# Optimization experiments

Measured on AMD Instinct MI355X. Metric: run time of the kernel, lower is better.

Reference implementation:

```python
import jax, jax.numpy as jnp
import numpy as np

NEG_BIG = -1e30  # stand-in for -inf in the log-space eps state


def wkv_scan(w, u, k, v, alpha0, beta0, eps0):
    """Numerically-stable RWKV WKV recurrence.

    w: exp(time_decay) (D,), u: time_first (D,)
    k, v: (B, T, D); alpha0, beta0, eps0: (B, D)
    Returns wkv (B, T, D) and final state.
    """
    def step(carry, kv_t):
        alpha, beta, eps = carry
        kt, vt = kv_t  # (B, D)
        # output: (e^{u+k} v + alpha) / (e^{u+k} + beta), stabilized
        ww = u + kt
        tau = jnp.maximum(eps, ww)
        e1 = jnp.exp(eps - tau)
        e2 = jnp.exp(ww - tau)
        out = (e1 * alpha + e2 * vt) / (e1 * beta + e2)
        # state update with decay: alpha' = e^{-w} alpha + e^{k} v (log-space)
        ww2 = eps - w
        tau2 = jnp.maximum(ww2, kt)
        e1b = jnp.exp(ww2 - tau2)
        e2b = jnp.exp(kt - tau2)
        return (e1b * alpha + e2b * vt, e1b * beta + e2b, tau2), out

    kT = jnp.swapaxes(k, 0, 1)  # (T, B, D)
    vT = jnp.swapaxes(v, 0, 1)
    (_, _, _), outs = jax.lax.scan(step, (alpha0, beta0, eps0), (kT, vT))
    return jnp.swapaxes(outs, 0, 1)  # (B, T, D)


def setup_inputs() -> dict:
    key = jax.random.key(0)
    ks = jax.random.split(key, 10)
    B, T, D = 4, 2048, 2048
    scale = 1.0 / np.sqrt(D)
    x = jax.random.normal(ks[0], (B, T, D), dtype=jnp.float32)
    time_decay = jax.random.uniform(ks[1], (D,), minval=-1.0, maxval=1.0)
    time_first = 0.1 * jax.random.normal(ks[2], (D,))
    time_mix_k = jax.random.uniform(ks[3], (1, 1, D))
    time_mix_v = jax.random.uniform(ks[4], (1, 1, D))
    time_mix_r = jax.random.uniform(ks[5], (1, 1, D))
    Wk = scale * jax.random.normal(ks[6], (D, D))
    Wv = scale * jax.random.normal(ks[7], (D, D))
    Wr = scale * jax.random.normal(ks[8], (D, D))
    Wo = scale * jax.random.normal(ks[9], (D, D))
    return {"x": x, "time_decay": time_decay, "time_first": time_first,
            "time_mix_k": time_mix_k, "time_mix_v": time_mix_v,
            "time_mix_r": time_mix_r, "Wk": Wk, "Wv": Wv, "Wr": Wr, "Wo": Wo}


def reference(x, time_decay, time_first, time_mix_k, time_mix_v, time_mix_r,
              Wk, Wv, Wr, Wo):
    B, T, D = x.shape
    # time_shift: prepend zero init_x, drop last token
    last_x = jnp.concatenate([jnp.zeros((B, 1, D), x.dtype), x[:, :-1, :]], axis=1)
    k = jnp.einsum('btd,ed->bte', x * time_mix_k + last_x * (1 - time_mix_k), Wk)
    v = jnp.einsum('btd,ed->bte', x * time_mix_v + last_x * (1 - time_mix_v), Wv)
    r = jnp.einsum('btd,ed->bte', x * time_mix_r + last_x * (1 - time_mix_r), Wr)
    sr = jax.nn.sigmoid(r)
    w = jnp.exp(time_decay)
    alpha0 = jnp.zeros((B, D), x.dtype)
    beta0 = jnp.zeros((B, D), x.dtype)
    eps0 = jnp.full((B, D), NEG_BIG, x.dtype)
    wkv = wkv_scan(w, time_first, k, v, alpha0, beta0, eps0)
    return jnp.einsum('btd,ed->bte', wkv * sr, Wo)
```

## Files before the change

### kernel.cpp

```cpp
#include <hip/hip_runtime.h>
#include <stdint.h>

typedef __bf16 bf16x8 __attribute__((ext_vector_type(8)));
typedef float f32x4 __attribute__((ext_vector_type(4)));

#define BM 128
#define BN 128
#define BK 64

__global__ void cvt_bf16(const float* __restrict__ in, __bf16* __restrict__ out,
                         long n) {
    long idx = ((long)blockIdx.x * blockDim.x + threadIdx.x) * 8;
    if (idx >= n) return;
    f32x4 a = *(const f32x4*)(in + idx);
    f32x4 b = *(const f32x4*)(in + idx + 4);
    bf16x8 o;
#pragma unroll
    for (int i = 0; i < 4; ++i) { o[i] = (__bf16)a[i]; o[i + 4] = (__bf16)b[i]; }
    *(bf16x8*)(out + idx) = o;
}

__global__ void mix_kernel(const float* __restrict__ x,
                           const float* __restrict__ mixw,
                           __bf16* __restrict__ out,
                           int T, int D, long total) {
    long idx = ((long)blockIdx.x * blockDim.x + threadIdx.x) * 8;
    if (idx >= total) return;
    int d = (int)(idx % D);
    long bt = idx / D;
    int t = (int)(bt % T);

    f32x4 x0 = *(const f32x4*)(x + idx);
    f32x4 x1 = *(const f32x4*)(x + idx + 4);
    f32x4 l0 = {}, l1 = {};
    if (t != 0) {
        l0 = *(const f32x4*)(x + idx - D);
        l1 = *(const f32x4*)(x + idx - D + 4);
    }
    f32x4 m0 = *(const f32x4*)(mixw + d);
    f32x4 m1 = *(const f32x4*)(mixw + d + 4);
    bf16x8 o;
#pragma unroll
    for (int i = 0; i < 4; ++i) {
        o[i]     = (__bf16)(x0[i] * m0[i] + l0[i] * (1.0f - m0[i]));
        o[i + 4] = (__bf16)(x1[i] * m1[i] + l1[i] * (1.0f - m1[i]));
    }
    *(bf16x8*)(out + idx) = o;
}

template <typename CT>
__global__ __launch_bounds__(256, 3)
void gemm_bt(const __bf16* __restrict__ A, const __bf16* __restrict__ Bt,
             CT* __restrict__ C, int M, int N, int K) {
    __shared__ __align__(16) __bf16 sA[BM * BK];
    __shared__ __align__(16) __bf16 sB[BN * BK];

    const int tid  = threadIdx.x;
    const int lane = tid & 63;
    const int wave = tid >> 6;
    const int m0 = blockIdx.y * BM;
    const int n0 = blockIdx.x * BN;
    const int wm = (wave & 1) * 64;
    const int wn = (wave >> 1) * 64;

    const int l8 = lane >> 3;
    const int c8 = lane & 7;
    const int cg = c8 ^ l8;

    const int q  = lane >> 4;
    const int ml = lane & 15;

    f32x4 acc[4][4] = {};

    for (int k0 = 0; k0 < K; k0 += BK) {
#pragma unroll
        for (int i = 0; i < 4; ++i) {
            const int cl  = wave * 4 + i;
            const int row = cl * 8 + l8;
            const __bf16* gA = A  + (long)(m0 + row) * K + (k0 + cg * 8);
            const __bf16* gB = Bt + (long)(n0 + row) * K + (k0 + cg * 8);
            __builtin_amdgcn_global_load_lds(
                (const __attribute__((address_space(1))) void*)gA,
                (__attribute__((address_space(3))) void*)(sA + cl * 512), 16, 0, 0);
            __builtin_amdgcn_global_load_lds(
                (const __attribute__((address_space(1))) void*)gB,
                (__attribute__((address_space(3))) void*)(sB + cl * 512), 16, 0, 0);
        }
        __syncthreads();

#pragma unroll
        for (int kk = 0; kk < BK; kk += 32) {
            bf16x8 af[4], bfr[4];
#pragma unroll
            for (int i = 0; i < 4; ++i) {
                int row = wm + i * 16 + ml;
                int cl  = ((kk >> 3) + q) ^ (row & 7);
                af[i] = *(const bf16x8*)(sA + row * BK + cl * 8);
            }
#pragma unroll
            for (int j = 0; j < 4; ++j) {
                int row = wn + j * 16 + ml;
                int cl  = ((kk >> 3) + q) ^ (row & 7);
                bfr[j] = *(const bf16x8*)(sB + row * BK + cl * 8);
            }
#pragma unroll
            for (int i = 0; i < 4; ++i)
#pragma unroll
                for (int j = 0; j < 4; ++j)
                    acc[i][j] = __builtin_amdgcn_mfma_f32_16x16x32_bf16(
                        af[i], bfr[j], acc[i][j], 0, 0, 0);
        }
        __syncthreads();
    }

#pragma unroll
    for (int i = 0; i < 4; ++i)
#pragma unroll
        for (int j = 0; j < 4; ++j)
#pragma unroll
            for (int rg = 0; rg < 4; ++rg) {
                int row = m0 + wm + i * 16 + q * 4 + rg;
                int col = n0 + wn + j * 16 + ml;
                C[(long)row * N + col] = (CT)acc[i][j][rg];
            }
}

template <typename ST>
__global__ void wkv_pass1(const ST* __restrict__ kk, const ST* __restrict__ vv,
                          const float* __restrict__ td,
                          float* __restrict__ al, float* __restrict__ bl,
                          float* __restrict__ el,
                          int Bn, int T, int D, int C, int L) {
    int gid = blockIdx.x * blockDim.x + threadIdx.x;
    int BD = Bn * D;
    if (gid >= BD * C) return;
    int c  = gid / BD;
    int bd = gid - c * BD;
    int b  = bd / D;
    int d  = bd - b * D;

    float w = __expf(td[d]);
    float alpha = 0.f, beta = 0.f, eps = -1e30f;
    long base = ((long)b * T + (long)c * L) * D + d;

    const int P = 8;
    float kb0[P], vb0[P], kb1[P], vb1[P];

    auto step = [&](float kt, float vt) {
        float ww2  = eps - w;
        float tau2 = fmaxf(ww2, kt);
        float e1b  = __expf(ww2 - tau2);
        float e2b  = __expf(kt - tau2);
        alpha = e1b * alpha + e2b * vt;
        beta  = e1b * beta + e2b;
        eps   = tau2;
    };

#pragma unroll
    for (int j = 0; j < P; ++j) {
        long o = base + (long)j * D;
        kb0[j] = (float)kk[o]; vb0[j] = (float)vv[o];
    }
    for (int t0 = 0; t0 < L; t0 += 2 * P) {
#pragma unroll
        for (int j = 0; j < P; ++j) {
            long o = base + (long)(t0 + P + j) * D;
            kb1[j] = (float)kk[o]; vb1[j] = (float)vv[o];
        }
#pragma unroll
        for (int j = 0; j < P; ++j) step(kb0[j], vb0[j]);
        if (t0 + 2 * P < L) {
#pragma unroll
            for (int j = 0; j < P; ++j) {
                long o = base + (long)(t0 + 2 * P + j) * D;
                kb0[j] = (float)kk[o]; vb0[j] = (float)vv[o];
            }
        }
#pragma unroll
        for (int j = 0; j < P; ++j) step(kb1[j], vb1[j]);
    }
    al[gid] = alpha; bl[gid] = beta; el[gid] = eps;
}

__global__ void wkv_combine(const float* __restrict__ al, const float* __restrict__ bl,
                            const float* __restrict__ el, const float* __restrict__ td,
                            float* __restrict__ ai, float* __restrict__ bi,
                            float* __restrict__ ei,
                            int Bn, int D, int C, int L) {
    int bd = blockIdx.x * blockDim.x + threadIdx.x;
    int BD = Bn * D;
    if (bd >= BD) return;
    int d = bd % D;
    float wL = __expf(td[d]) * (float)L;
    float a = 0.f, b2 = 0.f, e = -1e30f;
    for (int c = 0; c < C; ++c) {
        int idx = c * BD + bd;
        ai[idx] = a; bi[idx] = b2; ei[idx] = e;
        float ed  = e - wL;
        float la = al[idx], lb = bl[idx], le = el[idx];
        float tau = fmaxf(ed, le);
        float e1  = __expf(ed - tau);
        float e2  = __expf(le - tau);
        a  = a * e1 + la * e2;
        b2 = b2 * e1 + lb * e2;
        e  = tau;
    }
}

template <typename ST>
__global__ void wkv_pass2(const ST* __restrict__ kk, const ST* __restrict__ vv,
                          const __bf16* __restrict__ rr,
                          const float* __restrict__ td, const float* __restrict__ tf,
                          const float* __restrict__ ai, const float* __restrict__ bi,
                          const float* __restrict__ ei,
                          __bf16* __restrict__ out,
                          int Bn, int T, int D, int C, int L) {
    int gid = blockIdx.x * blockDim.x + threadIdx.x;
    int BD = Bn * D;
    if (gid >= BD * C) return;
    int c  = gid / BD;
    int bd = gid - c * BD;
    int b  = bd / D;
    int d  = bd - b * D;

    float u = tf[d];
    float w = __expf(td[d]);
    float alpha = ai[gid], beta = bi[gid], eps = ei[gid];
    long base = ((long)b * T + (long)c * L) * D + d;

    const int P = 8;
    float kb0[P], vb0[P], rb0[P], kb1[P], vb1[P], rb1[P];

    auto step = [&](float kt, float vt, float rt, int tIdx) {
        float ww  = u + kt;
        float tau = fmaxf(eps, ww);
        float e1  = __expf(eps - tau);
        float e2  = __expf(ww - tau);
        float num = e1 * alpha + e2 * vt;
        float den = e1 * beta + e2;
        float o_  = num * __builtin_amdgcn_rcpf(den);
        float ww2  = eps - w;
        float tau2 = fmaxf(ww2, kt);
        float e1b  = __expf(ww2 - tau2);
        float e2b  = __expf(kt - tau2);
        alpha = e1b * alpha + e2b * vt;
        beta  = e1b * beta + e2b;
        eps   = tau2;
        float sr = __builtin_amdgcn_rcpf(1.0f + __expf(-rt));
        out[base + (long)tIdx * D] = (__bf16)(o_ * sr);
    };

#pragma unroll
    for (int j = 0; j < P; ++j) {
        long o = base + (long)j * D;
        kb0[j] = (float)kk[o]; vb0[j] = (float)vv[o]; rb0[j] = (float)rr[o];
    }
    for (int t0 = 0; t0 < L; t0 += 2 * P) {
#pragma unroll
        for (int j = 0; j < P; ++j) {
            long o = base + (long)(t0 + P + j) * D;
            kb1[j] = (float)kk[o]; vb1[j] = (float)vv[o]; rb1[j] = (float)rr[o];
        }
#pragma unroll
        for (int j = 0; j < P; ++j) step(kb0[j], vb0[j], rb0[j], t0 + j);
        if (t0 + 2 * P < L) {
#pragma unroll
            for (int j = 0; j < P; ++j) {
                long o = base + (long)(t0 + 2 * P + j) * D;
                kb0[j] = (float)kk[o]; vb0[j] = (float)vv[o]; rb0[j] = (float)rr[o];
            }
        }
#pragma unroll
        for (int j = 0; j < P; ++j) step(kb1[j], vb1[j], rb1[j], t0 + P + j);
    }
}

extern "C" void kernel_launch(void* const* d_in, const int* in_sizes, int n_in,
                              void* d_out, int out_size, void* d_ws, size_t ws_size,
                              hipStream_t stream) {
    const float* x  = (const float*)d_in[0];
    const float* td = (const float*)d_in[1];
    const float* tf = (const float*)d_in[2];
    const float* mk = (const float*)d_in[3];
    const float* mv = (const float*)d_in[4];
    const float* mr = (const float*)d_in[5];
    const float* Wk = (const float*)d_in[6];
    const float* Wv = (const float*)d_in[7];
    const float* Wr = (const float*)d_in[8];
    const float* Wo = (const float*)d_in[9];
    float* out = (float*)d_out;

    const int D = in_sizes[1];
    const int T = 2048;
    const long total = (long)in_sizes[0];
    const int Bn = (int)(total / ((long)T * D));
    const int M = Bn * T;
    const int C = 32;
    const int L = T / C;
    const int BD = Bn * D;
    const int S = BD * C;

    char* p = (char*)d_ws;
    __bf16* xm  = (__bf16*)p;            p += total * 2;
    __bf16* wkb = (__bf16*)p;            p += (long)D * D * 2;
    __bf16* wvb = (__bf16*)p;            p += (long)D * D * 2;
    __bf16* wrb = (__bf16*)p;            p += (long)D * D * 2;
    __bf16* wob = (__bf16*)p;            p += (long)D * D * 2;
    size_t base_need = (size_t)(p - (char*)d_ws);
    bool use_f32 = ws_size >= base_need + (size_t)total * 4 * 2 + (size_t)total * 2;

    float* st = (float*)wkb;
    float *al = st, *bl = st + S, *el = st + 2 * S;
    float *ai = st + 3 * S, *bi = st + 4 * S, *ei = st + 5 * S;

    dim3 mixGrid((unsigned)((total / 8 + 255) / 256));
    dim3 cvtGrid((unsigned)(((long)D * D / 8 + 255) / 256));
    dim3 gemmGrid(D / BN, M / BM);
    dim3 p12Grid((S + 255) / 256);
    dim3 cmbGrid((BD + 255) / 256);

    cvt_bf16<<<cvtGrid, 256, 0, stream>>>(Wk, wkb, (long)D * D);
    cvt_bf16<<<cvtGrid, 256, 0, stream>>>(Wv, wvb, (long)D * D);
    cvt_bf16<<<cvtGrid, 256, 0, stream>>>(Wr, wrb, (long)D * D);
    cvt_bf16<<<cvtGrid, 256, 0, stream>>>(Wo, wob, (long)D * D);

    if (use_f32) {
        float*  kf = (float*)p;          p += total * 4;
        float*  vf = (float*)p;          p += total * 4;
        __bf16* rb = (__bf16*)p;

        mix_kernel<<<mixGrid, 256, 0, stream>>>(x, mk, xm, T, D, total);
        gemm_bt<float><<<gemmGrid, 256, 0, stream>>>(xm, wkb, kf, M, D, D);
        mix_kernel<<<mixGrid, 256, 0, stream>>>(x, mv, xm, T, D, total);
        gemm_bt<float><<<gemmGrid, 256, 0, stream>>>(xm, wvb, vf, M, D, D);
        mix_kernel<<<mixGrid, 256, 0, stream>>>(x, mr, xm, T, D, total);
        gemm_bt<__bf16><<<gemmGrid, 256, 0, stream>>>(xm, wrb, rb, M, D, D);

        wkv_pass1<float><<<p12Grid, 256, 0, stream>>>(kf, vf, td, al, bl, el,
                                                      Bn, T, D, C, L);
        wkv_combine<<<cmbGrid, 256, 0, stream>>>(al, bl, el, td, ai, bi, ei,
                                                 Bn, D, C, L);
        wkv_pass2<float><<<p12Grid, 256, 0, stream>>>(kf, vf, rb, td, tf,
                                                      ai, bi, ei, xm,
                                                      Bn, T, D, C, L);
        gemm_bt<float><<<gemmGrid, 256, 0, stream>>>(xm, wob, out, M, D, D);
    } else {
        __bf16* kb = (__bf16*)p;         p += total * 2;
        __bf16* vb = (__bf16*)p;         p += total * 2;
        __bf16* rb = (__bf16*)p;

        mix_kernel<<<mixGrid, 256, 0, stream>>>(x, mk, xm, T, D, total);
        gemm_bt<__bf16><<<gemmGrid, 256, 0, stream>>>(xm, wkb, kb, M, D, D);
        mix_kernel<<<mixGrid, 256, 0, stream>>>(x, mv, xm, T, D, total);
        gemm_bt<__bf16><<<gemmGrid, 256, 0, stream>>>(xm, wvb, vb, M, D, D);
        mix_kernel<<<mixGrid, 256, 0, stream>>>(x, mr, xm, T, D, total);
        gemm_bt<__bf16><<<gemmGrid, 256, 0, stream>>>(xm, wrb, rb, M, D, D);

        wkv_pass1<__bf16><<<p12Grid, 256, 0, stream>>>(kb, vb, td, al, bl, el,
                                                       Bn, T, D, C, L);
        wkv_combine<<<cmbGrid, 256, 0, stream>>>(al, bl, el, td, ai, bi, ei,
                                                 Bn, D, C, L);
        wkv_pass2<__bf16><<<p12Grid, 256, 0, stream>>>(kb, vb, rb, td, tf,
                                                       ai, bi, ei, xm,
                                                       Bn, T, D, C, L);
        gemm_bt<float><<<gemmGrid, 256, 0, stream>>>(xm, wob, out, M, D, D);
    }
}
```

Before: 584.6 us.

## Batch weight casts, fuse three token-mix passes, and launch V/R GEMMs together

Merges the four weight-conversion launches into one kernel and the three mix passes into one kernel that reads x once and writes three bf16 mixed inputs. The V and R projections now run as a single GEMM launch using a z-dimension of 2, which doubles the blocks available per launch. K stays fp32, V is now stored as bf16, and the workspace is re-laid out so K aliases the consumed mix buffers. This removes the ws-size-dependent fp32 path, lowers V precision, and relies on careful buffer aliasing.

```diff
diff --git a/kernel.cpp b/kernel.cpp
--- a/kernel.cpp
+++ b/kernel.cpp
@@ -8,22 +8,32 @@
 #define BN 128
 #define BK 64
 
-__global__ void cvt_bf16(const float* __restrict__ in, __bf16* __restrict__ out,
-                         long n) {
+__global__ void cvt4_bf16(const float* __restrict__ w0, const float* __restrict__ w1,
+                          const float* __restrict__ w2, const float* __restrict__ w3,
+                          __bf16* __restrict__ o0, __bf16* __restrict__ o1,
+                          __bf16* __restrict__ o2, __bf16* __restrict__ o3,
+                          long DD) {
     long idx = ((long)blockIdx.x * blockDim.x + threadIdx.x) * 8;
-    if (idx >= n) return;
-    f32x4 a = *(const f32x4*)(in + idx);
-    f32x4 b = *(const f32x4*)(in + idx + 4);
+    if (idx >= 4 * DD) return;
+    int w = (int)(idx / DD);
+    long off = idx - (long)w * DD;
+    const float* in = (w == 0) ? w0 : (w == 1) ? w1 : (w == 2) ? w2 : w3;
+    __bf16* out     = (w == 0) ? o0 : (w == 1) ? o1 : (w == 2) ? o2 : o3;
+    f32x4 a = *(const f32x4*)(in + off);
+    f32x4 b = *(const f32x4*)(in + off + 4);
     bf16x8 o;
 #pragma unroll
     for (int i = 0; i < 4; ++i) { o[i] = (__bf16)a[i]; o[i + 4] = (__bf16)b[i]; }
-    *(bf16x8*)(out + idx) = o;
-}
-
-__global__ void mix_kernel(const float* __restrict__ x,
-                           const float* __restrict__ mixw,
-                           __bf16* __restrict__ out,
-                           int T, int D, long total) {
+    *(bf16x8*)(out + off) = o;
+}
+
+__global__ void mix3_kernel(const float* __restrict__ x,
+                            const float* __restrict__ mk,
+                            const float* __restrict__ mv,
+                            const float* __restrict__ mr,
+                            __bf16* __restrict__ ok, __bf16* __restrict__ ov,
+                            __bf16* __restrict__ orr,
+                            int T, int D, long total) {
     long idx = ((long)blockIdx.x * blockDim.x + threadIdx.x) * 8;
     if (idx >= total) return;
     int d = (int)(idx % D);
@@ -37,21 +47,26 @@
         l0 = *(const f32x4*)(x + idx - D);
         l1 = *(const f32x4*)(x + idx - D + 4);
     }
-    f32x4 m0 = *(const f32x4*)(mixw + d);
-    f32x4 m1 = *(const f32x4*)(mixw + d + 4);
-    bf16x8 o;
-#pragma unroll
-    for (int i = 0; i < 4; ++i) {
-        o[i]     = (__bf16)(x0[i] * m0[i] + l0[i] * (1.0f - m0[i]));
-        o[i + 4] = (__bf16)(x1[i] * m1[i] + l1[i] * (1.0f - m1[i]));
-    }
-    *(bf16x8*)(out + idx) = o;
+    const float* mw[3] = {mk, mv, mr};
+    __bf16* ow[3] = {ok, ov, orr};
+#pragma unroll
+    for (int s = 0; s < 3; ++s) {
+        f32x4 m0 = *(const f32x4*)(mw[s] + d);
+        f32x4 m1 = *(const f32x4*)(mw[s] + d + 4);
+        bf16x8 o;
+#pragma unroll
+        for (int i = 0; i < 4; ++i) {
+            o[i]     = (__bf16)(x0[i] * m0[i] + l0[i] * (1.0f - m0[i]));
+            o[i + 4] = (__bf16)(x1[i] * m1[i] + l1[i] * (1.0f - m1[i]));
+        }
+        *(bf16x8*)(ow[s] + idx) = o;
+    }
 }
 
 template <typename CT>
-__global__ __launch_bounds__(256, 3)
-void gemm_bt(const __bf16* __restrict__ A, const __bf16* __restrict__ Bt,
-             CT* __restrict__ C, int M, int N, int K) {
+__device__ __attribute__((always_inline))
+void gemm_body(const __bf16* __restrict__ A, const __bf16* __restrict__ Bt,
+               CT* __restrict__ C, int M, int N, int K) {
     __shared__ __align__(16) __bf16 sA[BM * BK];
     __shared__ __align__(16) __bf16 sB[BN * BK];
 
@@ -125,8 +140,23 @@
             }
 }
 
-template <typename ST>
-__global__ void wkv_pass1(const ST* __restrict__ kk, const ST* __restrict__ vv,
+template <typename CT>
+__global__ __launch_bounds__(256, 3)
+void gemm_bt(const __bf16* __restrict__ A, const __bf16* __restrict__ Bt,
+             CT* __restrict__ C, int M, int N, int K) {
+    gemm_body<CT>(A, Bt, C, M, N, K);
+}
+
+__global__ __launch_bounds__(256, 3)
+void gemm_bt2(const __bf16* __restrict__ A0, const __bf16* __restrict__ A1,
+              const __bf16* __restrict__ B0, const __bf16* __restrict__ B1,
+              __bf16* __restrict__ C0, __bf16* __restrict__ C1,
+              int M, int N, int K) {
+    if (blockIdx.z == 0) gemm_body<__bf16>(A0, B0, C0, M, N, K);
+    else                 gemm_body<__bf16>(A1, B1, C1, M, N, K);
+}
+
+__global__ void wkv_pass1(const float* __restrict__ kk, const __bf16* __restrict__ vv,
                           const float* __restrict__ td,
                           float* __restrict__ al, float* __restrict__ bl,
                           float* __restrict__ el,
@@ -159,13 +189,13 @@
 #pragma unroll
     for (int j = 0; j < P; ++j) {
         long o = base + (long)j * D;
-        kb0[j] = (float)kk[o]; vb0[j] = (float)vv[o];
+        kb0[j] = kk[o]; vb0[j] = (float)vv[o];
     }
     for (int t0 = 0; t0 < L; t0 += 2 * P) {
 #pragma unroll
         for (int j = 0; j < P; ++j) {
             long o = base + (long)(t0 + P + j) * D;
-            kb1[j] = (float)kk[o]; vb1[j] = (float)vv[o];
+            kb1[j] = kk[o]; vb1[j] = (float)vv[o];
         }
 #pragma unroll
         for (int j = 0; j < P; ++j) step(kb0[j], vb0[j]);
@@ -173,7 +203,7 @@
 #pragma unroll
             for (int j = 0; j < P; ++j) {
                 long o = base + (long)(t0 + 2 * P + j) * D;
-                kb0[j] = (float)kk[o]; vb0[j] = (float)vv[o];
+                kb0[j] = kk[o]; vb0[j] = (float)vv[o];
             }
         }
 #pragma unroll
@@ -207,8 +237,7 @@
     }
 }
 
-template <typename ST>
-__global__ void wkv_pass2(const ST* __restrict__ kk, const ST* __restrict__ vv,
+__global__ void wkv_pass2(const float* __restrict__ kk, const __bf16* __restrict__ vv,
                           const __bf16* __restrict__ rr,
                           const float* __restrict__ td, const float* __restrict__ tf,
                           const float* __restrict__ ai, const float* __restrict__ bi,
@@ -253,13 +282,13 @@
 #pragma unroll
     for (int j = 0; j < P; ++j) {
         long o = base + (long)j * D;
-        kb0[j] = (float)kk[o]; vb0[j] = (float)vv[o]; rb0[j] = (float)rr[o];
+        kb0[j] = kk[o]; vb0[j] = (float)vv[o]; rb0[j] = (float)rr[o];
     }
     for (int t0 = 0; t0 < L; t0 += 2 * P) {
 #pragma unroll
         for (int j = 0; j < P; ++j) {
             long o = base + (long)(t0 + P + j) * D;
-            kb1[j] = (float)kk[o]; vb1[j] = (float)vv[o]; rb1[j] = (float)rr[o];
+            kb1[j] = kk[o]; vb1[j] = (float)vv[o]; rb1[j] = (float)rr[o];
         }
 #pragma unroll
         for (int j = 0; j < P; ++j) step(kb0[j], vb0[j], rb0[j], t0 + j);
@@ -267,7 +296,7 @@
 #pragma unroll
             for (int j = 0; j < P; ++j) {
                 long o = base + (long)(t0 + 2 * P + j) * D;
-                kb0[j] = (float)kk[o]; vb0[j] = (float)vv[o]; rb0[j] = (float)rr[o];
+                kb0[j] = kk[o]; vb0[j] = (float)vv[o]; rb0[j] = (float)rr[o];
             }
         }
 #pragma unroll
@@ -295,74 +324,46 @@
     const long total = (long)in_sizes[0];
     const int Bn = (int)(total / ((long)T * D));
     const int M = Bn * T;
+    const long DD = (long)D * D;
     const int C = 32;
     const int L = T / C;
     const int BD = Bn * D;
     const int S = BD * C;
 
     char* p = (char*)d_ws;
-    __bf16* xm  = (__bf16*)p;            p += total * 2;
-    __bf16* wkb = (__bf16*)p;            p += (long)D * D * 2;
-    __bf16* wvb = (__bf16*)p;            p += (long)D * D * 2;
-    __bf16* wrb = (__bf16*)p;            p += (long)D * D * 2;
-    __bf16* wob = (__bf16*)p;            p += (long)D * D * 2;
-    size_t base_need = (size_t)(p - (char*)d_ws);
-    bool use_f32 = ws_size >= base_need + (size_t)total * 4 * 2 + (size_t)total * 2;
-
-    float* st = (float*)wkb;
+    __bf16* xmk = (__bf16*)p;            p += total * 2;
+    __bf16* xmv = (__bf16*)p;            p += total * 2;
+    __bf16* xmr = (__bf16*)p;            p += total * 2;
+    __bf16* wkb = (__bf16*)p;            p += DD * 2;
+    __bf16* wvb = (__bf16*)p;            p += DD * 2;
+    __bf16* wrb = (__bf16*)p;            p += DD * 2;
+    __bf16* wob = (__bf16*)p;            p += DD * 2;
+    __bf16* vb  = (__bf16*)p;            p += total * 2;
+    __bf16* rb  = (__bf16*)p;            p += total * 2;
+
+    float*  kf = (float*)xmv;
+    __bf16* xo = xmk;
+    float*  st = (float*)wkb;
     float *al = st, *bl = st + S, *el = st + 2 * S;
     float *ai = st + 3 * S, *bi = st + 4 * S, *ei = st + 5 * S;
 
     dim3 mixGrid((unsigned)((total / 8 + 255) / 256));
-    dim3 cvtGrid((unsigned)(((long)D * D / 8 + 255) / 256));
+    dim3 cvtGrid((unsigned)((4 * DD / 8 + 255) / 256));
     dim3 gemmGrid(D / BN, M / BM);
+    dim3 gemm2Grid(D / BN, M / BM, 2);
     dim3 p12Grid((S + 255) / 256);
     dim3 cmbGrid((BD + 255) / 256);
 
-    cvt_bf16<<<cvtGrid, 256, 0, stream>>>(Wk, wkb, (long)D * D);
-    cvt_bf16<<<cvtGrid, 256, 0, stream>>>(Wv, wvb, (long)D * D);
-    cvt_bf16<<<cvtGrid, 256, 0, stream>>>(Wr, wrb, (long)D * D);
-    cvt_bf16<<<cvtGrid, 256, 0, stream>>>(Wo, wob, (long)D * D);
-
-    if (use_f32) {
-        float*  kf = (float*)p;          p += total * 4;
-        float*  vf = (float*)p;          p += total * 4;
-        __bf16* rb = (__bf16*)p;
-
-        mix_kernel<<<mixGrid, 256, 0, stream>>>(x, mk, xm, T, D, total);
-        gemm_bt<float><<<gemmGrid, 256, 0, stream>>>(xm, wkb, kf, M, D, D);
-        mix_kernel<<<mixGrid, 256, 0, stream>>>(x, mv, xm, T, D, total);
-        gemm_bt<float><<<gemmGrid, 256, 0, stream>>>(xm, wvb, vf, M, D, D);
-        mix_kernel<<<mixGrid, 256, 0, stream>>>(x, mr, xm, T, D, total);
-        gemm_bt<__bf16><<<gemmGrid, 256, 0, stream>>>(xm, wrb, rb, M, D, D);
-
-        wkv_pass1<float><<<p12Grid, 256, 0, stream>>>(kf, vf, td, al, bl, el,
-                                                      Bn, T, D, C, L);
-        wkv_combine<<<cmbGrid, 256, 0, stream>>>(al, bl, el, td, ai, bi, ei,
-                                                 Bn, D, C, L);
-        wkv_pass2<float><<<p12Grid, 256, 0, stream>>>(kf, vf, rb, td, tf,
-                                                      ai, bi, ei, xm,
-                                                      Bn, T, D, C, L);
-        gemm_bt<float><<<gemmGrid, 256, 0, stream>>>(xm, wob, out, M, D, D);
-    } else {
-        __bf16* kb = (__bf16*)p;         p += total * 2;
-        __bf16* vb = (__bf16*)p;         p += total * 2;
-        __bf16* rb = (__bf16*)p;
-
-        mix_kernel<<<mixGrid, 256, 0, stream>>>(x, mk, xm, T, D, total);
-        gemm_bt<__bf16><<<gemmGrid, 256, 0, stream>>>(xm, wkb, kb, M, D, D);
-        mix_kernel<<<mixGrid, 256, 0, stream>>>(x, mv, xm, T, D, total);
-        gemm_bt<__bf16><<<gemmGrid, 256, 0, stream>>>(xm, wvb, vb, M, D, D);
-        mix_kernel<<<mixGrid, 256, 0, stream>>>(x, mr, xm, T, D, total);
-        gemm_bt<__bf16><<<gemmGrid, 256, 0, stream>>>(xm, wrb, rb, M, D, D);
-
-        wkv_pass1<__bf16><<<p12Grid, 256, 0, stream>>>(kb, vb, td, al, bl, el,
-                                                       Bn, T, D, C, L);
-        wkv_combine<<<cmbGrid, 256, 0, stream>>>(al, bl, el, td, ai, bi, ei,
-                                                 Bn, D, C, L);
-        wkv_pass2<__bf16><<<p12Grid, 256, 0, stream>>>(kb, vb, rb, td, tf,
-                                                       ai, bi, ei, xm,
-                                                       Bn, T, D, C, L);
-        gemm_bt<float><<<gemmGrid, 256, 0, stream>>>(xm, wob, out, M, D, D);
-    }
-}
+    cvt4_bf16<<<cvtGrid, 256, 0, stream>>>(Wk, Wv, Wr, Wo, wkb, wvb, wrb, wob, DD);
+    mix3_kernel<<<mixGrid, 256, 0, stream>>>(x, mk, mv, mr, xmk, xmv, xmr, T, D, total);
+
+    gemm_bt2<<<gemm2Grid, 256, 0, stream>>>(xmv, xmr, wvb, wrb, vb, rb, M, D, D);
+    gemm_bt<float><<<gemmGrid, 256, 0, stream>>>(xmk, wkb, kf, M, D, D);
+
+    wkv_pass1<<<p12Grid, 256, 0, stream>>>(kf, vb, td, al, bl, el, Bn, T, D, C, L);
+    wkv_combine<<<cmbGrid, 256, 0, stream>>>(al, bl, el, td, ai, bi, ei, Bn, D, C, L);
+    wkv_pass2<<<p12Grid, 256, 0, stream>>>(kf, vb, rb, td, tf, ai, bi, ei, xo,
+                                           Bn, T, D, C, L);
+
+    gemm_bt<float><<<gemmGrid, 256, 0, stream>>>(xo, wob, out, M, D, D);
+}
```

Measured after the change: 544.3 us. 1.07x faster.
